# Kernel optimization log

Measured on AMD Instinct MI355X. Metric: run time of the kernel, lower is better.

Reference implementation:

```python
import jax, jax.numpy as jnp
import numpy as np

N_NODES = 100000
N_EDGES = 1600000
IN_C, HID, OUT_C = 128, 64, 64
N_LAYERS = 16
ALPHA, THETA = 0.1, 0.5


def setup_inputs() -> dict:
    key = jax.random.key(0)
    ks = jax.random.split(key, 8)
    x = jax.random.normal(ks[0], (N_NODES, IN_C), dtype=jnp.float32)
    edge_index = jax.random.randint(ks[1], (2, N_EDGES), 0, N_NODES, dtype=jnp.int64)
    # torch Linear: weight [out, in], bias [out]
    lin0_w = jax.random.normal(ks[2], (HID, IN_C), dtype=jnp.float32) / np.sqrt(IN_C)
    lin0_b = jnp.zeros((HID,), dtype=jnp.float32)
    lin1_w = jax.random.normal(ks[3], (OUT_C, HID), dtype=jnp.float32) / np.sqrt(HID)
    lin1_b = jnp.zeros((OUT_C,), dtype=jnp.float32)
    # GCN2Conv weight1 per layer: [HID, HID], applied as h @ W
    conv_w = jax.random.normal(ks[4], (N_LAYERS, HID, HID), dtype=jnp.float32) / np.sqrt(HID)
    return {"x": x, "edge_index": edge_index, "lin0_w": lin0_w, "lin0_b": lin0_b,
            "lin1_w": lin1_w, "lin1_b": lin1_b, "conv_w": conv_w}


def reference(x, edge_index, lin0_w, lin0_b, lin1_w, lin1_b, conv_w):
    src, dst = edge_index[0], edge_index[1]
    # input projection (dropout p=0 in eval -> identity)
    h = jax.nn.relu(x @ lin0_w.T + lin0_b)  # [N, HID]
    h0 = h
    for l in range(N_LAYERS):
        # unweighted sum aggregation over edges (normalize=False, edge_weight=None)
        agg = jax.ops.segment_sum(h[src], dst, num_segments=N_NODES)  # [N, HID]
        z = (1.0 - ALPHA) * agg + ALPHA * h0  # initial residual
        beta = np.log(THETA / (l + 1) + 1.0).astype(np.float32)  # identity mapping strength
        h = jax.nn.relu((1.0 - beta) * z + beta * (z @ conv_w[l]))
    return h @ lin1_w.T + lin1_b  # [N, OUT_C]
```

## Files before the change

kernel.cpp:

```cpp
#include <hip/hip_runtime.h>
#include <cmath>

#define HID 64
#define IN_C 128

__device__ __forceinline__ float rl(float v, int k) {
    return __uint_as_float(__builtin_amdgcn_readlane(__float_as_uint(v), k));
}
__device__ __forceinline__ float bflo(unsigned u) { return __uint_as_float(u << 16); }
__device__ __forceinline__ float bfhi(unsigned u) { return __uint_as_float(u & 0xffff0000u); }
__device__ __forceinline__ unsigned bfpack(float lo, float hi) {
    unsigned a = __float_as_uint(lo), b = __float_as_uint(hi);
    a = (a + 0x7fffu + ((a >> 16) & 1u)) >> 16;
    b = (b + 0x7fffu + ((b >> 16) & 1u)) & 0xffff0000u;
    return a | b;
}

__device__ __forceinline__ float xadd8(float x) {
    int t = __builtin_amdgcn_update_dpp(0, __float_as_int(x), 0x128, 0xF, 0xF, true);
    return x + __int_as_float(t);
}
#if __has_builtin(__builtin_amdgcn_permlane16_swap)
typedef unsigned uvec2 __attribute__((ext_vector_type(2)));
__device__ __forceinline__ float xadd16(float x) {
    uvec2 r = __builtin_amdgcn_permlane16_swap(__float_as_uint(x), __float_as_uint(x), false, false);
    return __uint_as_float(r[0]) + __uint_as_float(r[1]);
}
#else
__device__ __forceinline__ float xadd16(float x) { return x + __shfl_xor(x, 16); }
#endif
#if __has_builtin(__builtin_amdgcn_permlane32_swap)
typedef unsigned uvec2b __attribute__((ext_vector_type(2)));
__device__ __forceinline__ float xadd32(float x) {
    uvec2b r = __builtin_amdgcn_permlane32_swap(__float_as_uint(x), __float_as_uint(x), false, false);
    return __uint_as_float(r[0]) + __uint_as_float(r[1]);
}
#else
__device__ __forceinline__ float xadd32(float x) { return x + __shfl_xor(x, 32); }
#endif
__device__ __forceinline__ float pairswap(float x) {
    int t = __builtin_amdgcn_update_dpp(0, __float_as_int(x), 0xB1, 0xF, 0xF, true);
    return __int_as_float(t);
}


__global__ void k_hist(const int* __restrict__ dst, int* __restrict__ counts, int E) {
    int e = blockIdx.x * blockDim.x + threadIdx.x;
    if (e < E) atomicAdd(&counts[dst[e]], 1);
}

__global__ void k_scan_block(const int* __restrict__ counts, int* __restrict__ row_ptr,
                             int* __restrict__ chunk_sums, int n) {
    __shared__ int s[1024];
    int i = blockIdx.x * 1024 + threadIdx.x;
    int v = (i < n) ? counts[i] : 0;
    s[threadIdx.x] = v;
    __syncthreads();
    for (int off = 1; off < 1024; off <<= 1) {
        int t = (threadIdx.x >= off) ? s[threadIdx.x - off] : 0;
        __syncthreads();
        s[threadIdx.x] += t;
        __syncthreads();
    }
    if (i < n) row_ptr[i] = s[threadIdx.x] - v;
    if (threadIdx.x == 1023) chunk_sums[blockIdx.x] = s[1023];
}

__global__ void k_scan_fix(int* __restrict__ row_ptr, const int* __restrict__ chunk_sums,
                           int n, int total) {
    __shared__ int base_s;
    if (threadIdx.x == 0) {
        int b = 0;
        for (int c = 0; c < (int)blockIdx.x; ++c) b += chunk_sums[c];
        base_s = b;
    }
    __syncthreads();
    int i = blockIdx.x * 1024 + threadIdx.x;
    if (i < n) row_ptr[i] += base_s;
    if (i == 0) row_ptr[n] = total;
}

__global__ void k_fill(const int* __restrict__ src, const int* __restrict__ dst,
                       const int* __restrict__ row_ptr, int* __restrict__ cursor,
                       int* __restrict__ col_idx, int E) {
    int e = blockIdx.x * blockDim.x + threadIdx.x;
    if (e < E) {
        int d = dst[e];
        int pos = row_ptr[d] + atomicAdd(&cursor[d], 1);
        col_idx[pos] = src[e];
    }
}

__global__ __launch_bounds__(256) void k_lin0(const float* __restrict__ x,
                                              const float* __restrict__ w,
                                              const float* __restrict__ b,
                                              unsigned* __restrict__ h0, int N) {
    __shared__ float Wt[IN_C * 65];
    for (int i = threadIdx.x; i < IN_C * HID; i += 256) {
        int o = i >> 7, k = i & 127;
        Wt[k * 65 + o] = w[i];
    }
    __syncthreads();
    int lane = threadIdx.x & 63;
    int wid = (blockIdx.x * blockDim.x + threadIdx.x) >> 6;
    int nw = (gridDim.x * blockDim.x) >> 6;
    float bias = b[lane];
    for (int n0 = wid; n0 < N; n0 += 2 * nw) {
        int n1 = n0 + nw;
        bool v1 = n1 < N;
        int n1c = v1 ? n1 : n0;
        float xa0 = x[(size_t)n0 * IN_C + lane];
        float xa1 = x[(size_t)n0 * IN_C + 64 + lane];
        float xb0 = x[(size_t)n1c * IN_C + lane];
        float xb1 = x[(size_t)n1c * IN_C + 64 + lane];
        float acc0 = bias, acc1 = bias;
#pragma unroll
        for (int k = 0; k < 64; ++k) {
            float wv = Wt[k * 65 + lane];
            acc0 = fmaf(rl(xa0, k), wv, acc0);
            acc1 = fmaf(rl(xb0, k), wv, acc1);
        }
#pragma unroll
        for (int k = 0; k < 64; ++k) {
            float wv = Wt[(64 + k) * 65 + lane];
            acc0 = fmaf(rl(xa1, k), wv, acc0);
            acc1 = fmaf(rl(xb1, k), wv, acc1);
        }
        acc0 = fmaxf(acc0, 0.f);
        acc1 = fmaxf(acc1, 0.f);
        float p0 = pairswap(acc0);
        float p1 = pairswap(acc1);
        if ((lane & 1) == 0) {
            h0[(size_t)n0 * 32 + (lane >> 1)] = bfpack(acc0, p0);
            if (v1) h0[(size_t)n1 * 32 + (lane >> 1)] = bfpack(acc1, p1);
        }
    }
}

__global__ __launch_bounds__(256) void k_layer(const uint4* __restrict__ hin,
                                               const uint4* __restrict__ h0,
                                               unsigned* __restrict__ hout,
                                               const float* __restrict__ W,
                                               const int* __restrict__ row_ptr,
                                               const int* __restrict__ col_idx,
                                               float beta, int N) {
    __shared__ uint2 Wp[16 * 64];
    __shared__ float zb[4 * 64];
    for (int idx = threadIdx.x; idx < 16 * 64; idx += 256) {
        int k4 = idx >> 6, c = idx & 63;
        float w0 = W[(4 * k4 + 0) * 64 + c];
        float w1 = W[(4 * k4 + 1) * 64 + c];
        float w2 = W[(4 * k4 + 2) * 64 + c];
        float w3 = W[(4 * k4 + 3) * 64 + c];
        uint2 p;
        p.x = bfpack(w0, w1);
        p.y = bfpack(w2, w3);
        Wp[idx] = p;
    }
    __syncthreads();

    int lane = threadIdx.x & 63;
    int wslot = threadIdx.x >> 6;
    int sub = lane >> 3;
    int cg = lane & 7;
    int wid = (blockIdx.x * blockDim.x + threadIdx.x) >> 6;
    int nw = (gridDim.x * blockDim.x) >> 6;

    for (int n = wid; n < N; n += nw) {
        int b = row_ptr[n];
        int d = row_ptr[n + 1] - b;
        float a[8];
#pragma unroll
        for (int c = 0; c < 8; ++c) a[c] = 0.f;
        int j = 0;
        for (; j + 16 <= d; j += 16) {
            int i0 = col_idx[b + j + sub];
            int i1 = col_idx[b + j + 8 + sub];
            uint4 q0 = hin[(size_t)i0 * 8 + cg];
            uint4 q1 = hin[(size_t)i1 * 8 + cg];
            a[0] += bflo(q0.x); a[1] += bfhi(q0.x);
            a[2] += bflo(q0.y); a[3] += bfhi(q0.y);
            a[4] += bflo(q0.z); a[5] += bfhi(q0.z);
            a[6] += bflo(q0.w); a[7] += bfhi(q0.w);
            a[0] += bflo(q1.x); a[1] += bfhi(q1.x);
            a[2] += bflo(q1.y); a[3] += bfhi(q1.y);
            a[4] += bflo(q1.z); a[5] += bfhi(q1.z);
            a[6] += bflo(q1.w); a[7] += bfhi(q1.w);
        }
        if (j + sub < d) {
            int i0 = col_idx[b + j + sub];
            uint4 q0 = hin[(size_t)i0 * 8 + cg];
            a[0] += bflo(q0.x); a[1] += bfhi(q0.x);
            a[2] += bflo(q0.y); a[3] += bfhi(q0.y);
            a[4] += bflo(q0.z); a[5] += bfhi(q0.z);
            a[6] += bflo(q0.w); a[7] += bfhi(q0.w);
        }
        if (j + 8 + sub < d) {
            int i1 = col_idx[b + j + 8 + sub];
            uint4 q1 = hin[(size_t)i1 * 8 + cg];
            a[0] += bflo(q1.x); a[1] += bfhi(q1.x);
            a[2] += bflo(q1.y); a[3] += bfhi(q1.y);
            a[4] += bflo(q1.z); a[5] += bfhi(q1.z);
            a[6] += bflo(q1.w); a[7] += bfhi(q1.w);
        }
#pragma unroll
        for (int c = 0; c < 8; ++c) a[c] = xadd8(a[c]);
#pragma unroll
        for (int c = 0; c < 8; ++c) a[c] = xadd16(a[c]);
#pragma unroll
        for (int c = 0; c < 8; ++c) a[c] = xadd32(a[c]);

        uint4 hq = h0[(size_t)n * 8 + cg];
        float z[8];
        z[0] = 0.9f * a[0] + 0.1f * bflo(hq.x);
        z[1] = 0.9f * a[1] + 0.1f * bfhi(hq.x);
        z[2] = 0.9f * a[2] + 0.1f * bflo(hq.y);
        z[3] = 0.9f * a[3] + 0.1f * bfhi(hq.y);
        z[4] = 0.9f * a[4] + 0.1f * bflo(hq.z);
        z[5] = 0.9f * a[5] + 0.1f * bfhi(hq.z);
        z[6] = 0.9f * a[6] + 0.1f * bflo(hq.w);
        z[7] = 0.9f * a[7] + 0.1f * bfhi(hq.w);

        if (sub == 0) {
            float4 zlo = make_float4(z[0], z[1], z[2], z[3]);
            float4 zhi = make_float4(z[4], z[5], z[6], z[7]);
            *(float4*)&zb[wslot * 64 + cg * 8]     = zlo;
            *(float4*)&zb[wslot * 64 + cg * 8 + 4] = zhi;
        }
        float zl = zb[wslot * 64 + lane];

        float g0 = 0.f, g1 = 0.f, g2 = 0.f, g3 = 0.f;
#pragma unroll
        for (int k4 = 0; k4 < 16; ++k4) {
            uint2 wp = Wp[k4 * 64 + lane];
            int k = 4 * k4;
            g0 = fmaf(rl(z[(k + 0) & 7], (k + 0) >> 3), bflo(wp.x), g0);
            g1 = fmaf(rl(z[(k + 1) & 7], (k + 1) >> 3), bfhi(wp.x), g1);
            g2 = fmaf(rl(z[(k + 2) & 7], (k + 2) >> 3), bflo(wp.y), g2);
            g3 = fmaf(rl(z[(k + 3) & 7], (k + 3) >> 3), bfhi(wp.y), g3);
        }
        float g = (g0 + g1) + (g2 + g3);

        float r = fmaxf((1.f - beta) * zl + beta * g, 0.f);
        float rn = pairswap(r);
        if ((lane & 1) == 0) hout[(size_t)n * 32 + (lane >> 1)] = bfpack(r, rn);
    }
}

__global__ __launch_bounds__(256) void k_lin1(const unsigned* __restrict__ h,
                                              const float* __restrict__ w,
                                              const float* __restrict__ b,
                                              float* __restrict__ out, int N) {
    __shared__ float Wt[HID * 65];
    for (int i = threadIdx.x; i < HID * HID; i += 256) {
        int o = i >> 6, k = i & 63;
        Wt[k * 65 + o] = w[i];
    }
    __syncthreads();
    int lane = threadIdx.x & 63;
    int wid = (blockIdx.x * blockDim.x + threadIdx.x) >> 6;
    int nw = (gridDim.x * blockDim.x) >> 6;
    float bias = b[lane];
    for (int n0 = wid; n0 < N; n0 += 2 * nw) {
        int n1 = n0 + nw;
        bool v1 = n1 < N;
        int n1c = v1 ? n1 : n0;
        unsigned ua = h[(size_t)n0 * 32 + (lane >> 1)];
        unsigned ub = h[(size_t)n1c * 32 + (lane >> 1)];
        float ha = (lane & 1) ? bfhi(ua) : bflo(ua);
        float hb = (lane & 1) ? bfhi(ub) : bflo(ub);
        float acc0 = bias, acc1 = bias;
#pragma unroll
        for (int k = 0; k < 64; ++k) {
            float wv = Wt[k * 65 + lane];
            acc0 = fmaf(rl(ha, k), wv, acc0);
            acc1 = fmaf(rl(hb, k), wv, acc1);
        }
        out[(size_t)n0 * HID + lane] = acc0;
        if (v1) out[(size_t)n1 * HID + lane] = acc1;
    }
}

extern "C" void kernel_launch(void* const* d_in, const int* in_sizes, int n_in,
                              void* d_out, int out_size, void* d_ws, size_t ws_size,
                              hipStream_t stream) {
    const float* x      = (const float*)d_in[0];
    const int*   ei     = (const int*)d_in[1];
    const float* lin0_w = (const float*)d_in[2];
    const float* lin0_b = (const float*)d_in[3];
    const float* lin1_w = (const float*)d_in[4];
    const float* lin1_b = (const float*)d_in[5];
    const float* conv_w = (const float*)d_in[6];

    int N = in_sizes[0] / IN_C;
    int E = in_sizes[1] / 2;
    const int* src = ei;
    const int* dst = ei + E;

    unsigned* h0 = (unsigned*)d_ws;
    unsigned* hA = h0 + (size_t)N * 32;
    unsigned* hB = hA + (size_t)N * 32;
    int* row_ptr    = (int*)(hB + (size_t)N * 32);
    int* cursor     = row_ptr + (N + 1);
    int* col_idx    = cursor + N;
    int* chunk_sums = col_idx + E;

    int nch = (N + 1023) / 1024;

    hipMemsetAsync(cursor, 0, (size_t)N * sizeof(int), stream);
    k_hist<<<(E + 255) / 256, 256, 0, stream>>>(dst, cursor, E);
    k_scan_block<<<nch, 1024, 0, stream>>>(cursor, row_ptr, chunk_sums, N);
    k_scan_fix<<<nch, 1024, 0, stream>>>(row_ptr, chunk_sums, N, E);
    hipMemsetAsync(cursor, 0, (size_t)N * sizeof(int), stream);
    k_fill<<<(E + 255) / 256, 256, 0, stream>>>(src, dst, row_ptr, cursor, col_idx, E);

    k_lin0<<<1024, 256, 0, stream>>>(x, lin0_w, lin0_b, h0, N);

    const unsigned* cur = h0;
    for (int l = 0; l < 16; ++l) {
        float beta = (float)log(0.5 / (double)(l + 1) + 1.0);
        unsigned* nxt = (l & 1) ? hB : hA;
        k_layer<<<2048, 256, 0, stream>>>((const uint4*)cur, (const uint4*)h0, nxt,
                                          conv_w + (size_t)l * HID * HID,
                                          row_ptr, col_idx, beta, N);
        cur = nxt;
    }

    k_lin1<<<1024, 256, 0, stream>>>(cur, lin1_w, lin1_b, (float*)d_out, N);
}
```

Before: 1.511 ms.

## Process two nodes per wavefront and fold identity blend into bf16 weights

Each wavefront now gathers and transforms two destination nodes per iteration, with clamped index loads and masking instead of tail branches, so more independent memory requests are in flight. The (1-beta)I + beta*W blend is folded into the shared bf16 weight matrix. This removes the per-node shared-memory z staging and the separate residual mix. Weights are packed 8 per uint4 to halve LDS loads. The cost is higher register pressure, wasted masked loads when the two nodes' degrees differ, and extra bf16 rounding on the diagonal terms.

```diff
diff --git a/kernel.cpp b/kernel.cpp
--- a/kernel.cpp
+++ b/kernel.cpp
@@ -137,113 +137,133 @@
     }
 }
 
+__device__ __forceinline__ void mask4(uint4& q, bool v) {
+    q.x = v ? q.x : 0u; q.y = v ? q.y : 0u; q.z = v ? q.z : 0u; q.w = v ? q.w : 0u;
+}
+__device__ __forceinline__ void acc8(float* a, const uint4& q) {
+    a[0] += bflo(q.x); a[1] += bfhi(q.x);
+    a[2] += bflo(q.y); a[3] += bfhi(q.y);
+    a[4] += bflo(q.z); a[5] += bfhi(q.z);
+    a[6] += bflo(q.w); a[7] += bfhi(q.w);
+}
+
 __global__ __launch_bounds__(256) void k_layer(const uint4* __restrict__ hin,
                                                const uint4* __restrict__ h0,
                                                unsigned* __restrict__ hout,
                                                const float* __restrict__ W,
                                                const int* __restrict__ row_ptr,
                                                const int* __restrict__ col_idx,
-                                               float beta, int N) {
-    __shared__ uint2 Wp[16 * 64];
-    __shared__ float zb[4 * 64];
-    for (int idx = threadIdx.x; idx < 16 * 64; idx += 256) {
-        int k4 = idx >> 6, c = idx & 63;
-        float w0 = W[(4 * k4 + 0) * 64 + c];
-        float w1 = W[(4 * k4 + 1) * 64 + c];
-        float w2 = W[(4 * k4 + 2) * 64 + c];
-        float w3 = W[(4 * k4 + 3) * 64 + c];
-        uint2 p;
-        p.x = bfpack(w0, w1);
-        p.y = bfpack(w2, w3);
+                                               float beta, int N, int E) {
+    __shared__ uint4 Wp[8 * 64];
+    for (int idx = threadIdx.x; idx < 8 * 64; idx += 256) {
+        int k8 = idx >> 6, c = idx & 63;
+        float wv[8];
+#pragma unroll
+        for (int m = 0; m < 8; ++m) {
+            int k = 8 * k8 + m;
+            float v = beta * W[k * 64 + c];
+            if (k == c) v += 1.f - beta;
+            wv[m] = v;
+        }
+        uint4 p;
+        p.x = bfpack(wv[0], wv[1]); p.y = bfpack(wv[2], wv[3]);
+        p.z = bfpack(wv[4], wv[5]); p.w = bfpack(wv[6], wv[7]);
         Wp[idx] = p;
     }
     __syncthreads();
 
     int lane = threadIdx.x & 63;
-    int wslot = threadIdx.x >> 6;
     int sub = lane >> 3;
     int cg = lane & 7;
     int wid = (blockIdx.x * blockDim.x + threadIdx.x) >> 6;
     int nw = (gridDim.x * blockDim.x) >> 6;
 
-    for (int n = wid; n < N; n += nw) {
-        int b = row_ptr[n];
-        int d = row_ptr[n + 1] - b;
-        float a[8];
-#pragma unroll
-        for (int c = 0; c < 8; ++c) a[c] = 0.f;
-        int j = 0;
-        for (; j + 16 <= d; j += 16) {
-            int i0 = col_idx[b + j + sub];
-            int i1 = col_idx[b + j + 8 + sub];
-            uint4 q0 = hin[(size_t)i0 * 8 + cg];
-            uint4 q1 = hin[(size_t)i1 * 8 + cg];
-            a[0] += bflo(q0.x); a[1] += bfhi(q0.x);
-            a[2] += bflo(q0.y); a[3] += bfhi(q0.y);
-            a[4] += bflo(q0.z); a[5] += bfhi(q0.z);
-            a[6] += bflo(q0.w); a[7] += bfhi(q0.w);
-            a[0] += bflo(q1.x); a[1] += bfhi(q1.x);
-            a[2] += bflo(q1.y); a[3] += bfhi(q1.y);
-            a[4] += bflo(q1.z); a[5] += bfhi(q1.z);
-            a[6] += bflo(q1.w); a[7] += bfhi(q1.w);
-        }
-        if (j + sub < d) {
-            int i0 = col_idx[b + j + sub];
-            uint4 q0 = hin[(size_t)i0 * 8 + cg];
-            a[0] += bflo(q0.x); a[1] += bfhi(q0.x);
-            a[2] += bflo(q0.y); a[3] += bfhi(q0.y);
-            a[4] += bflo(q0.z); a[5] += bfhi(q0.z);
-            a[6] += bflo(q0.w); a[7] += bfhi(q0.w);
-        }
-        if (j + 8 + sub < d) {
-            int i1 = col_idx[b + j + 8 + sub];
-            uint4 q1 = hin[(size_t)i1 * 8 + cg];
-            a[0] += bflo(q1.x); a[1] += bfhi(q1.x);
-            a[2] += bflo(q1.y); a[3] += bfhi(q1.y);
-            a[4] += bflo(q1.z); a[5] += bfhi(q1.z);
-            a[6] += bflo(q1.w); a[7] += bfhi(q1.w);
-        }
-#pragma unroll
-        for (int c = 0; c < 8; ++c) a[c] = xadd8(a[c]);
-#pragma unroll
-        for (int c = 0; c < 8; ++c) a[c] = xadd16(a[c]);
-#pragma unroll
-        for (int c = 0; c < 8; ++c) a[c] = xadd32(a[c]);
-
-        uint4 hq = h0[(size_t)n * 8 + cg];
-        float z[8];
-        z[0] = 0.9f * a[0] + 0.1f * bflo(hq.x);
-        z[1] = 0.9f * a[1] + 0.1f * bfhi(hq.x);
-        z[2] = 0.9f * a[2] + 0.1f * bflo(hq.y);
-        z[3] = 0.9f * a[3] + 0.1f * bfhi(hq.y);
-        z[4] = 0.9f * a[4] + 0.1f * bflo(hq.z);
-        z[5] = 0.9f * a[5] + 0.1f * bfhi(hq.z);
-        z[6] = 0.9f * a[6] + 0.1f * bflo(hq.w);
-        z[7] = 0.9f * a[7] + 0.1f * bfhi(hq.w);
-
-        if (sub == 0) {
-            float4 zlo = make_float4(z[0], z[1], z[2], z[3]);
-            float4 zhi = make_float4(z[4], z[5], z[6], z[7]);
-            *(float4*)&zb[wslot * 64 + cg * 8]     = zlo;
-            *(float4*)&zb[wslot * 64 + cg * 8 + 4] = zhi;
-        }
-        float zl = zb[wslot * 64 + lane];
-
-        float g0 = 0.f, g1 = 0.f, g2 = 0.f, g3 = 0.f;
-#pragma unroll
-        for (int k4 = 0; k4 < 16; ++k4) {
-            uint2 wp = Wp[k4 * 64 + lane];
-            int k = 4 * k4;
-            g0 = fmaf(rl(z[(k + 0) & 7], (k + 0) >> 3), bflo(wp.x), g0);
-            g1 = fmaf(rl(z[(k + 1) & 7], (k + 1) >> 3), bfhi(wp.x), g1);
-            g2 = fmaf(rl(z[(k + 2) & 7], (k + 2) >> 3), bflo(wp.y), g2);
-            g3 = fmaf(rl(z[(k + 3) & 7], (k + 3) >> 3), bfhi(wp.y), g3);
-        }
-        float g = (g0 + g1) + (g2 + g3);
-
-        float r = fmaxf((1.f - beta) * zl + beta * g, 0.f);
-        float rn = pairswap(r);
-        if ((lane & 1) == 0) hout[(size_t)n * 32 + (lane >> 1)] = bfpack(r, rn);
+    for (int n = wid; n < N; n += 2 * nw) {
+        int nB = n + nw;
+        bool vB = nB < N;
+        int nBc = vB ? nB : n;
+        int bA = row_ptr[n];
+        int dA = row_ptr[n + 1] - bA;
+        int bB = row_ptr[nBc];
+        int dB = vB ? row_ptr[nBc + 1] - bB : 0;
+        uint4 hqA = h0[(size_t)n * 8 + cg];
+        uint4 hqB = h0[(size_t)nBc * 8 + cg];
+        int lastA = max(bA + dA - 1, 0);
+        int lastB = max(bB + dB - 1, 0);
+        float aA[8], aB[8];
+#pragma unroll
+        for (int c = 0; c < 8; ++c) { aA[c] = 0.f; aB[c] = 0.f; }
+        int rmax = max(dA, dB);
+        for (int j = 0; j < rmax; j += 16) {
+            int p0 = j + sub, p1 = j + 8 + sub;
+            int iA0 = col_idx[min(bA + p0, lastA)];
+            int iA1 = col_idx[min(bA + p1, lastA)];
+            int iB0 = col_idx[min(bB + p0, lastB)];
+            int iB1 = col_idx[min(bB + p1, lastB)];
+            uint4 qA0 = hin[(size_t)iA0 * 8 + cg];
+            uint4 qA1 = hin[(size_t)iA1 * 8 + cg];
+            uint4 qB0 = hin[(size_t)iB0 * 8 + cg];
+            uint4 qB1 = hin[(size_t)iB1 * 8 + cg];
+            mask4(qA0, p0 < dA); mask4(qA1, p1 < dA);
+            mask4(qB0, p0 < dB); mask4(qB1, p1 < dB);
+            acc8(aA, qA0); acc8(aA, qA1);
+            acc8(aB, qB0); acc8(aB, qB1);
+        }
+#pragma unroll
+        for (int c = 0; c < 8; ++c) { aA[c] = xadd8(aA[c]);  aB[c] = xadd8(aB[c]); }
+#pragma unroll
+        for (int c = 0; c < 8; ++c) { aA[c] = xadd16(aA[c]); aB[c] = xadd16(aB[c]); }
+#pragma unroll
+        for (int c = 0; c < 8; ++c) { aA[c] = xadd32(aA[c]); aB[c] = xadd32(aB[c]); }
+
+        float zA[8], zB[8];
+        zA[0] = 0.9f * aA[0] + 0.1f * bflo(hqA.x);
+        zA[1] = 0.9f * aA[1] + 0.1f * bfhi(hqA.x);
+        zA[2] = 0.9f * aA[2] + 0.1f * bflo(hqA.y);
+        zA[3] = 0.9f * aA[3] + 0.1f * bfhi(hqA.y);
+        zA[4] = 0.9f * aA[4] + 0.1f * bflo(hqA.z);
+        zA[5] = 0.9f * aA[5] + 0.1f * bfhi(hqA.z);
+        zA[6] = 0.9f * aA[6] + 0.1f * bflo(hqA.w);
+        zA[7] = 0.9f * aA[7] + 0.1f * bfhi(hqA.w);
+        zB[0] = 0.9f * aB[0] + 0.1f * bflo(hqB.x);
+        zB[1] = 0.9f * aB[1] + 0.1f * bfhi(hqB.x);
+        zB[2] = 0.9f * aB[2] + 0.1f * bflo(hqB.y);
+        zB[3] = 0.9f * aB[3] + 0.1f * bfhi(hqB.y);
+        zB[4] = 0.9f * aB[4] + 0.1f * bflo(hqB.z);
+        zB[5] = 0.9f * aB[5] + 0.1f * bfhi(hqB.z);
+        zB[6] = 0.9f * aB[6] + 0.1f * bflo(hqB.w);
+        zB[7] = 0.9f * aB[7] + 0.1f * bfhi(hqB.w);
+
+        float gA0 = 0.f, gA1 = 0.f, gA2 = 0.f, gA3 = 0.f;
+        float gB0 = 0.f, gB1 = 0.f, gB2 = 0.f, gB3 = 0.f;
+#pragma unroll
+        for (int k8 = 0; k8 < 8; ++k8) {
+            uint4 wp = Wp[k8 * 64 + lane];
+            gA0 = fmaf(rl(zA[0], k8), bflo(wp.x), gA0);
+            gA1 = fmaf(rl(zA[1], k8), bfhi(wp.x), gA1);
+            gA2 = fmaf(rl(zA[2], k8), bflo(wp.y), gA2);
+            gA3 = fmaf(rl(zA[3], k8), bfhi(wp.y), gA3);
+            gA0 = fmaf(rl(zA[4], k8), bflo(wp.z), gA0);
+            gA1 = fmaf(rl(zA[5], k8), bfhi(wp.z), gA1);
+            gA2 = fmaf(rl(zA[6], k8), bflo(wp.w), gA2);
+            gA3 = fmaf(rl(zA[7], k8), bfhi(wp.w), gA3);
+            gB0 = fmaf(rl(zB[0], k8), bflo(wp.x), gB0);
+            gB1 = fmaf(rl(zB[1], k8), bfhi(wp.x), gB1);
+            gB2 = fmaf(rl(zB[2], k8), bflo(wp.y), gB2);
+            gB3 = fmaf(rl(zB[3], k8), bfhi(wp.y), gB3);
+            gB0 = fmaf(rl(zB[4], k8), bflo(wp.z), gB0);
+            gB1 = fmaf(rl(zB[5], k8), bfhi(wp.z), gB1);
+            gB2 = fmaf(rl(zB[6], k8), bflo(wp.w), gB2);
+            gB3 = fmaf(rl(zB[7], k8), bfhi(wp.w), gB3);
+        }
+        float rA = fmaxf((gA0 + gA1) + (gA2 + gA3), 0.f);
+        float rB = fmaxf((gB0 + gB1) + (gB2 + gB3), 0.f);
+        float rAn = pairswap(rA);
+        float rBn = pairswap(rB);
+        if ((lane & 1) == 0) {
+            hout[(size_t)n * 32 + (lane >> 1)] = bfpack(rA, rAn);
+            if (vB) hout[(size_t)nB * 32 + (lane >> 1)] = bfpack(rB, rBn);
+        }
     }
 }
 
@@ -322,7 +342,7 @@
         unsigned* nxt = (l & 1) ? hB : hA;
         k_layer<<<2048, 256, 0, stream>>>((const uint4*)cur, (const uint4*)h0, nxt,
                                           conv_w + (size_t)l * HID * HID,
-                                          row_ptr, col_idx, beta, N);
+                                          row_ptr, col_idx, beta, N, E);
         cur = nxt;
     }
 
```

New measurement: 1.507 ms. No clear change (-0.3%).
